# Performance work log

Measured on AMD Instinct MI355X. Metric: run time of the kernel, lower is better.

The kernel has to match this reference:

```python
import jax, jax.numpy as jnp
import numpy as np

Q_DIM = 9   # state(7) + action(2)
KV_DIM = 5  # fixed by get_input_tensors: 4 relative features + r_trans
H = 3
D = KV_DIM * H  # 15


def setup_inputs() -> dict:
    key = jax.random.key(0)
    ks = jax.random.split(key, 16)
    b, t = 32, 256

    def u(k, shape, fan_in):
        lim = (1.0 / fan_in) ** 0.5
        return jax.random.uniform(k, shape, jnp.float32, -lim, lim)

    return {
        "state": jax.random.normal(ks[0], (b, t, 7), jnp.float32),
        "action": jax.random.normal(ks[1], (b, t, 2), jnp.float32),
        "Wk": u(ks[2], (D, KV_DIM), KV_DIM),
        "Wq": u(ks[3], (D, Q_DIM), Q_DIM),
        "Wv": u(ks[4], (D, KV_DIM), KV_DIM),
        "att_bias": jax.random.uniform(ks[5], (KV_DIM,), jnp.float32, -0.1, 0.1),
        "Wscore": u(ks[6], (1, KV_DIM), KV_DIM),
        "bscore": u(ks[7], (1,), KV_DIM),
        "g1": jnp.ones((D,), jnp.float32),
        "beta1": jnp.zeros((D,), jnp.float32),
        "W1": u(ks[8], (5 * D, D), D),
        "bff1": u(ks[9], (5 * D,), D),
        "W2": u(ks[10], (D, 5 * D), 5 * D),
        "bff2": u(ks[11], (D,), 5 * D),
        "g2": jnp.ones((D,), jnp.float32),
        "beta2": jnp.zeros((D,), jnp.float32),
    }


def _layernorm(x, g, b, eps=1e-5):
    m = jnp.mean(x, axis=-1, keepdims=True)
    v = jnp.var(x, axis=-1, keepdims=True)
    return (x - m) * jax.lax.rsqrt(v + eps) * g + b


def _get_input_tensors(state):
    b, t, _ = state.shape
    init = state[..., :4]                                  # (b,t,4)
    rel = init[:, None, :, :] - init[:, :, None, :]        # (b,t,t,4): row i, col j -> s_j - s_i
    xy = rel.reshape(b, t, t, 2, 2).transpose(0, 1, 2, 4, 3)  # [...,0,:]=(x,vx), [...,1,:]=(y,vy)
    ang = -state[..., -1] + 0.5 * jnp.pi                   # (b,t)
    c = jnp.cos(ang)[:, None, :, None]                     # broadcast over row dim -> angle of col j
    s = jnp.sin(ang)[:, None, :, None]
    xr = xy[..., 0, :] * c - xy[..., 1, :] * s             # (b,t,t,2)
    yr = xy[..., 0, :] * s + xy[..., 1, :] * c
    rel = jnp.concatenate([xr, yr], axis=3)                # [xn,vxn,yn,vyn]
    rel = rel.reshape(b, t, t, 2, 2).transpose(0, 1, 2, 4, 3).reshape(b, t, t, 4)  # [xn,yn,vxn,vyn]
    # drop diagonal (j != i) via precomputed off-diagonal column indices
    rows = jnp.arange(t)[:, None]
    j = jnp.arange(t - 1)[None, :]
    cols = j + (j >= rows)                                 # (t,t-1)
    rel = rel[:, rows, cols, :]                            # (b,t,t-1,4)
    r = jnp.sqrt(rel[..., 0] ** 2 + rel[..., 1] ** 2)[..., None]  # (b,t,t-1,1)
    r_trans = 1.0 / (1.0 + jnp.exp(-1.0 + 5.0 * (r - 0.2)))
    kv_x = jnp.concatenate([rel[..., :2] / r, rel[..., 2:], r_trans], axis=-1)  # (b,t,t-1,5)
    return state, kv_x


def reference(state, action, Wk, Wq, Wv, att_bias, Wscore, bscore,
              g1, beta1, W1, bff1, W2, bff2, g2, beta2):
    q_x, kv_x = _get_input_tensors(state)
    q_x = jnp.concatenate([q_x, action], axis=-1)          # (b,t,Q_DIM)
    b, t, tm1, _ = kv_x.shape

    keys = (kv_x @ Wk.T).reshape(b, t, tm1, H, KV_DIM)     # (b,t,t-1,h,k)
    queries = (q_x @ Wq.T).reshape(b, t, 1, H, KV_DIM)
    e = jnp.tanh(keys + queries + att_bias)
    score = (e @ Wscore.T + bscore)[..., 0]                # (b,t,t-1,h)
    values = (kv_x @ Wv.T).reshape(b, t, tm1, H, KV_DIM)
    w = jax.nn.softmax(score, axis=2)                      # softmax over the t-1 neighbours
    x = jnp.einsum('btjh,btjhk->bthk', w, values).reshape(b, t, H * KV_DIM)

    x = _layernorm(x, g1, beta1)
    y = jax.nn.relu(x @ W1.T + bff1) @ W2.T + bff2
    x = x + y
    return _layernorm(x, g2, beta2)
```

## Files before the change

### kernel.cpp

```cpp
#include <hip/hip_runtime.h>
#include <math.h>

#define TT   256
#define TM1  255
#define QD   9
#define KD   5
#define NH   3
#define DD   15
#define HID  75
#define NR   18

#define K2E  2.8853900817779268f
#define L2E  1.4426950408889634f
#define INVK 0.34657359027997264f

typedef float v2f __attribute__((ext_vector_type(2)));

__device__ __forceinline__ v2f v2splat(float s) { v2f r; r.x = s; r.y = s; return r; }

__device__ __forceinline__ float fast_rcp(float x) {
    return __builtin_amdgcn_rcpf(x);
}

__device__ __forceinline__ float exp2_raw(float x) {
    float r; asm("v_exp_f32 %0, %1" : "=v"(r) : "v"(x)); return r;
}

template<int CTRL>
__device__ __forceinline__ float dpp_add(float x) {
    int y = __builtin_amdgcn_update_dpp(0, __float_as_int(x), CTRL, 0xf, 0xf, true);
    return x + __int_as_float(y);
}

__device__ __forceinline__ float wave_sum63(float x) {
    x = dpp_add<0x111>(x);
    x = dpp_add<0x112>(x);
    x = dpp_add<0x114>(x);
    x = dpp_add<0x118>(x);
    x = dpp_add<0x142>(x);
    x = dpp_add<0x143>(x);
    return x;
}

__device__ __forceinline__ float bcast(float x, int l) {
    return __int_as_float(__builtin_amdgcn_readlane(__float_as_int(x), l));
}

__global__ __launch_bounds__(256, 8)
void fused_block_kernel(const float* __restrict__ state,
                        const float* __restrict__ action,
                        const float* __restrict__ Wk,
                        const float* __restrict__ Wq,
                        const float* __restrict__ Wv,
                        const float* __restrict__ att_bias,
                        const float* __restrict__ Wscore,
                        const float* __restrict__ bscore,
                        const float* __restrict__ g1,
                        const float* __restrict__ beta1,
                        const float* __restrict__ W1,
                        const float* __restrict__ bff1,
                        const float* __restrict__ W2,
                        const float* __restrict__ bff2,
                        const float* __restrict__ g2,
                        const float* __restrict__ beta2,
                        float* __restrict__ out)
{
    const int tid  = threadIdx.x;
    const int lane = tid & 63;
    const int wv   = __builtin_amdgcn_readfirstlane(tid >> 6);
    const int qgrp = blockIdx.x * 4 + wv;
    const int b    = qgrp >> 8;
    const int qi   = qgrp & 255;

    __shared__ __align__(16) float s_wk8[DD*8];
    __shared__ float s_h[4][76];

    const float* __restrict__ sb  = state + (size_t)b*TT*7;
    const float* __restrict__ sti = sb + qi*7;
    const float si0 = sti[0], si1 = sti[1], si2 = sti[2], si3 = sti[3];

    if (tid < DD) {
        #pragma unroll
        for (int c = 0; c < KD; c++) s_wk8[tid*8+c] = Wk[tid*KD+c];
        s_wk8[tid*8+5] = -K2E * Wscore[tid % KD];
        s_wk8[tid*8+6] = 0.0f;
        s_wk8[tid*8+7] = 0.0f;
    }

    float qv = 0.0f;
    if (lane < DD) {
        float acc = att_bias[lane % KD];
        #pragma unroll
        for (int k = 0; k < 7; k++) acc = fmaf(Wq[lane*QD+k], sti[k], acc);
        acc = fmaf(Wq[lane*QD+7], action[((size_t)b*TT+qi)*2 + 0], acc);
        acc = fmaf(Wq[lane*QD+8], action[((size_t)b*TT+qi)*2 + 1], acc);
        qv = acc * K2E;
    }
    float qb2[DD];
    #pragma unroll
    for (int d = 0; d < DD; d++) qb2[d] = bcast(qv, d);

    float Cn = bscore[0];
    #pragma unroll
    for (int kk = 0; kk < KD; kk++) Cn += Wscore[kk];
    const float C2 = L2E * Cn;

    __syncthreads();

    float red[NR];
    #pragma unroll
    for (int n = 0; n < NR; n++) red[n] = 0.0f;

    #pragma unroll
    for (int g = 0; g < 2; g++) {
        const int mm0 = lane + g*128;
        const int mm1 = mm0 + 64;
        const int jj0 = mm0 + (mm0 >= qi ? 1 : 0);
        int       jj1 = mm1 + (mm1 >= qi ? 1 : 0);
        jj1 = (jj1 < TT) ? jj1 : (TT-1);
        const float* __restrict__ r0 = sb + jj0*7;
        const float* __restrict__ r1 = sb + jj1*7;

        v2f d0, d1, d2, d3, th;
        d0.x = r0[0]; d0.y = r1[0];
        d1.x = r0[1]; d1.y = r1[1];
        d2.x = r0[2]; d2.y = r1[2];
        d3.x = r0[3]; d3.y = r1[3];
        th.x = r0[6]; th.y = r1[6];
        d0 = d0 - v2splat(si0);
        d1 = d1 - v2splat(si1);
        d2 = d2 - v2splat(si2);
        d3 = d3 - v2splat(si3);

        v2f cs, sn;
        cs.x = __sinf(th.x); cs.y = __sinf(th.y);
        sn.x = __cosf(th.x); sn.y = __cosf(th.y);

        v2f xr0 = d0*cs - d1*sn;
        v2f yr0 = d0*sn + d1*cs;
        v2f xr1 = d2*cs - d3*sn;
        v2f yr1 = d2*sn + d3*cs;
        v2f s2  = xr0*xr0 + yr0*yr0;
        s2.x = fmaxf(s2.x, 1e-12f);
        s2.y = fmaxf(s2.y, 1e-12f);
        v2f rinv;
        rinv.x = __builtin_amdgcn_rsqf(s2.x);
        rinv.y = __builtin_amdgcn_rsqf(s2.y);
        v2f r = s2 * rinv;
        v2f ea;
        ea.x = exp2_raw(fmaf(7.213475204444817f, r.x, -2.8853900817779268f));
        ea.y = exp2_raw(fmaf(7.213475204444817f, r.y, -2.8853900817779268f));
        v2f rt;
        rt.x = fast_rcp(1.0f + ea.x);
        rt.y = fast_rcp(1.0f + ea.y);

        v2f t  = v2splat(K2E) * rinv;
        const v2f F0 = t * xr0;
        const v2f F1 = t * yr0;
        const v2f F2 = v2splat(K2E) * xr1;
        const v2f F3 = v2splat(K2E) * yr1;
        const v2f F4 = v2splat(K2E) * rt;

        v2f Cp;
        Cp.x = (mm0 < TM1) ? C2 : -100.0f;
        Cp.y = (mm1 < TM1) ? C2 : -100.0f;

        #pragma unroll
        for (int h = 0; h < NH; h++) {
            v2f sc = Cp;
            #pragma unroll
            for (int kk = 0; kk < KD; kk++) {
                const int d = h*KD + kk;
                const float4 wA = *(const float4*)&s_wk8[d*8];
                const float2 wB = *(const float2*)&s_wk8[d*8+4];

                v2f a = v2splat(qb2[d]);
                a = a + v2splat(wA.x) * F0;
                a = a + v2splat(wA.y) * F1;
                a = a + v2splat(wA.z) * F2;
                a = a + v2splat(wA.w) * F3;
                a = a + v2splat(wB.x) * F4;
                v2f e, sg;
                e.x = exp2_raw(a.x);
                e.y = exp2_raw(a.y);
                sg.x = fast_rcp(e.x + 1.0f);
                sg.y = fast_rcp(e.y + 1.0f);
                sc = sc + v2splat(wB.y) * sg;
            }
            v2f p;
            p.x = exp2_raw(sc.x);
            p.y = exp2_raw(sc.y);
            red[h] += p.x + p.y;
            red[NH+h*KD+0] = fmaf(p.y, F0.y, fmaf(p.x, F0.x, red[NH+h*KD+0]));
            red[NH+h*KD+1] = fmaf(p.y, F1.y, fmaf(p.x, F1.x, red[NH+h*KD+1]));
            red[NH+h*KD+2] = fmaf(p.y, F2.y, fmaf(p.x, F2.x, red[NH+h*KD+2]));
            red[NH+h*KD+3] = fmaf(p.y, F3.y, fmaf(p.x, F3.x, red[NH+h*KD+3]));
            red[NH+h*KD+4] = fmaf(p.y, F4.y, fmaf(p.x, F4.x, red[NH+h*KD+4]));
        }
    }

    #pragma unroll
    for (int n = 0; n < NR; n++) red[n] = wave_sum63(red[n]);
    float fin[NR];
    #pragma unroll
    for (int n = 0; n < NR; n++) fin[n] = bcast(red[n], 63);

    float xm = 0.0f;
    if (lane < DD) {
        const int h = lane / KD;
        float acc = 0.0f;
        #pragma unroll
        for (int c = 0; c < KD; c++) acc = fmaf(Wv[lane*KD+c], fin[NH+h*KD+c], acc);
        xm = acc * fast_rcp(fin[h]) * INVK;
    }

    float s1 = xm, sq = xm*xm;
    #pragma unroll
    for (int off = 8; off >= 1; off >>= 1) {
        s1 += __shfl_xor(s1, off, 16);
        sq += __shfl_xor(sq, off, 16);
    }
    const float mu1   = s1 * (1.0f/DD);
    const float rstd1 = rsqrtf(sq * (1.0f/DD) - mu1*mu1 + 1e-5f);
    float xln = 0.0f;
    if (lane < DD) xln = (xm - mu1) * rstd1 * g1[lane] + beta1[lane];

    float xs[DD];
    #pragma unroll
    for (int d = 0; d < DD; d++) xs[d] = bcast(xln, d);

    {
        float h0 = bff1[lane];
        #pragma unroll
        for (int k = 0; k < DD; k++) h0 = fmaf(W1[lane*DD+k], xs[k], h0);
        s_h[wv][lane] = fmaxf(h0, 0.0f);
        if (lane < HID-64) {
            float h1 = bff1[lane+64];
            #pragma unroll
            for (int k = 0; k < DD; k++) h1 = fmaf(W1[(lane+64)*DD+k], xs[k], h1);
            s_h[wv][lane+64] = fmaxf(h1, 0.0f);
        }
    }

    const int c2  = lane >> 4;
    const int d2c = lane & 15;
    const int cc  = (c2 < 3) ? c2 : 2;
    const int dc  = (d2c < DD) ? d2c : 0;
    float acc2 = 0.0f;
    #pragma unroll
    for (int k = 0; k < 25; k++)
        acc2 = fmaf(W2[dc*HID + cc*25 + k], s_h[wv][cc*25 + k], acc2);
    acc2 = (c2 < 3) ? acc2 : 0.0f;
    acc2 += __shfl_xor(acc2, 16);
    acc2 += __shfl_xor(acc2, 32);

    float x2 = 0.0f;
    if (lane < DD) x2 = xln + bff2[lane] + acc2;
    float t1 = x2, t2 = x2*x2;
    #pragma unroll
    for (int off = 8; off >= 1; off >>= 1) {
        t1 += __shfl_xor(t1, off, 16);
        t2 += __shfl_xor(t2, off, 16);
    }
    const float mu2   = t1 * (1.0f/DD);
    const float rstd2 = rsqrtf(t2 * (1.0f/DD) - mu2*mu2 + 1e-5f);
    if (lane < DD)
        out[(size_t)qgrp*DD + lane] = (x2 - mu2) * rstd2 * g2[lane] + beta2[lane];
}

extern "C" void kernel_launch(void* const* d_in, const int* in_sizes, int n_in,
                              void* d_out, int out_size, void* d_ws, size_t ws_size,
                              hipStream_t stream) {
    const float* state    = (const float*)d_in[0];
    const float* action   = (const float*)d_in[1];
    const float* Wk       = (const float*)d_in[2];
    const float* Wq       = (const float*)d_in[3];
    const float* Wv       = (const float*)d_in[4];
    const float* att_bias = (const float*)d_in[5];
    const float* Wscore   = (const float*)d_in[6];
    const float* bscore   = (const float*)d_in[7];
    const float* g1       = (const float*)d_in[8];
    const float* beta1    = (const float*)d_in[9];
    const float* W1       = (const float*)d_in[10];
    const float* bff1     = (const float*)d_in[11];
    const float* W2       = (const float*)d_in[12];
    const float* bff2     = (const float*)d_in[13];
    const float* g2       = (const float*)d_in[14];
    const float* beta2    = (const float*)d_in[15];
    float* out = (float*)d_out;

    dim3 grid(32 * 256 / 4);
    dim3 block(256);
    fused_block_kernel<<<grid, block, 0, stream>>>(
        state, action, Wk, Wq, Wv, att_bias, Wscore, bscore,
        g1, beta1, W1, bff1, W2, bff2, g2, beta2, out);
}
```

Measured before the change: 29.17 us.

## Split each query's neighbour loop across two waves with LDS reduction

New measurement: 29.28 us. About the same (+0.4%).

```diff
diff --git a/kernel.cpp b/kernel.cpp
--- a/kernel.cpp
+++ b/kernel.cpp
@@ -46,7 +46,7 @@
     return __int_as_float(__builtin_amdgcn_readlane(__float_as_int(x), l));
 }
 
-__global__ __launch_bounds__(256, 8)
+__global__ __launch_bounds__(256)
 void fused_block_kernel(const float* __restrict__ state,
                         const float* __restrict__ action,
                         const float* __restrict__ Wk,
@@ -68,12 +68,15 @@
     const int tid  = threadIdx.x;
     const int lane = tid & 63;
     const int wv   = __builtin_amdgcn_readfirstlane(tid >> 6);
-    const int qgrp = blockIdx.x * 4 + wv;
+    const int qloc = wv >> 1;
+    const int half = wv & 1;
+    const int qgrp = blockIdx.x * 2 + qloc;
     const int b    = qgrp >> 8;
     const int qi   = qgrp & 255;
 
     __shared__ __align__(16) float s_wk8[DD*8];
-    __shared__ float s_h[4][76];
+    __shared__ float s_red[2][2][NR];
+    __shared__ float s_h[2][76];
 
     const float* __restrict__ sb  = state + (size_t)b*TT*7;
     const float* __restrict__ sti = sb + qi*7;
@@ -107,13 +110,9 @@
 
     __syncthreads();
 
-    float red[NR];
-    #pragma unroll
-    for (int n = 0; n < NR; n++) red[n] = 0.0f;
-
-    #pragma unroll
-    for (int g = 0; g < 2; g++) {
-        const int mm0 = lane + g*128;
+    v2f F0, F1, F2, F3, F4, Cp;
+    {
+        const int mm0 = half*128 + lane;
         const int mm1 = mm0 + 64;
         const int jj0 = mm0 + (mm0 >= qi ? 1 : 0);
         int       jj1 = mm1 + (mm1 >= qi ? 1 : 0);
@@ -154,56 +153,67 @@
         rt.x = fast_rcp(1.0f + ea.x);
         rt.y = fast_rcp(1.0f + ea.y);
 
-        v2f t  = v2splat(K2E) * rinv;
-        const v2f F0 = t * xr0;
-        const v2f F1 = t * yr0;
-        const v2f F2 = v2splat(K2E) * xr1;
-        const v2f F3 = v2splat(K2E) * yr1;
-        const v2f F4 = v2splat(K2E) * rt;
-
-        v2f Cp;
+        v2f t = v2splat(K2E) * rinv;
+        F0 = t * xr0;
+        F1 = t * yr0;
+        F2 = v2splat(K2E) * xr1;
+        F3 = v2splat(K2E) * yr1;
+        F4 = v2splat(K2E) * rt;
+
         Cp.x = (mm0 < TM1) ? C2 : -100.0f;
         Cp.y = (mm1 < TM1) ? C2 : -100.0f;
-
-        #pragma unroll
-        for (int h = 0; h < NH; h++) {
-            v2f sc = Cp;
-            #pragma unroll
-            for (int kk = 0; kk < KD; kk++) {
-                const int d = h*KD + kk;
-                const float4 wA = *(const float4*)&s_wk8[d*8];
-                const float2 wB = *(const float2*)&s_wk8[d*8+4];
-
-                v2f a = v2splat(qb2[d]);
-                a = a + v2splat(wA.x) * F0;
-                a = a + v2splat(wA.y) * F1;
-                a = a + v2splat(wA.z) * F2;
-                a = a + v2splat(wA.w) * F3;
-                a = a + v2splat(wB.x) * F4;
-                v2f e, sg;
-                e.x = exp2_raw(a.x);
-                e.y = exp2_raw(a.y);
-                sg.x = fast_rcp(e.x + 1.0f);
-                sg.y = fast_rcp(e.y + 1.0f);
-                sc = sc + v2splat(wB.y) * sg;
-            }
-            v2f p;
-            p.x = exp2_raw(sc.x);
-            p.y = exp2_raw(sc.y);
-            red[h] += p.x + p.y;
-            red[NH+h*KD+0] = fmaf(p.y, F0.y, fmaf(p.x, F0.x, red[NH+h*KD+0]));
-            red[NH+h*KD+1] = fmaf(p.y, F1.y, fmaf(p.x, F1.x, red[NH+h*KD+1]));
-            red[NH+h*KD+2] = fmaf(p.y, F2.y, fmaf(p.x, F2.x, red[NH+h*KD+2]));
-            red[NH+h*KD+3] = fmaf(p.y, F3.y, fmaf(p.x, F3.x, red[NH+h*KD+3]));
-            red[NH+h*KD+4] = fmaf(p.y, F4.y, fmaf(p.x, F4.x, red[NH+h*KD+4]));
+    }
+
+    float red[NR];
+    #pragma unroll
+    for (int n = 0; n < NR; n++) red[n] = 0.0f;
+
+    #pragma unroll
+    for (int h = 0; h < NH; h++) {
+        v2f sc = Cp;
+        #pragma unroll
+        for (int kk = 0; kk < KD; kk++) {
+            const int d = h*KD + kk;
+            const float4 wA = *(const float4*)&s_wk8[d*8];
+            const float2 wB = *(const float2*)&s_wk8[d*8+4];
+
+            v2f a = v2splat(qb2[d]);
+            a = a + v2splat(wA.x) * F0;
+            a = a + v2splat(wA.y) * F1;
+            a = a + v2splat(wA.z) * F2;
+            a = a + v2splat(wA.w) * F3;
+            a = a + v2splat(wB.x) * F4;
+            v2f e, sg;
+            e.x = exp2_raw(a.x);
+            e.y = exp2_raw(a.y);
+            sg.x = fast_rcp(e.x + 1.0f);
+            sg.y = fast_rcp(e.y + 1.0f);
+            sc = sc + v2splat(wB.y) * sg;
         }
+        v2f p;
+        p.x = exp2_raw(sc.x);
+        p.y = exp2_raw(sc.y);
+        red[h] += p.x + p.y;
+        red[NH+h*KD+0] = fmaf(p.y, F0.y, fmaf(p.x, F0.x, red[NH+h*KD+0]));
+        red[NH+h*KD+1] = fmaf(p.y, F1.y, fmaf(p.x, F1.x, red[NH+h*KD+1]));
+        red[NH+h*KD+2] = fmaf(p.y, F2.y, fmaf(p.x, F2.x, red[NH+h*KD+2]));
+        red[NH+h*KD+3] = fmaf(p.y, F3.y, fmaf(p.x, F3.x, red[NH+h*KD+3]));
+        red[NH+h*KD+4] = fmaf(p.y, F4.y, fmaf(p.x, F4.x, red[NH+h*KD+4]));
     }
 
     #pragma unroll
     for (int n = 0; n < NR; n++) red[n] = wave_sum63(red[n]);
+    if (lane == 63) {
+        #pragma unroll
+        for (int n = 0; n < NR; n++) s_red[qloc][half][n] = red[n];
+    }
+    __syncthreads();
+    if (half == 1) return;
+
     float fin[NR];
     #pragma unroll
-    for (int n = 0; n < NR; n++) fin[n] = bcast(red[n], 63);
+    for (int n = 0; n < NR; n++)
+        fin[n] = s_red[qloc][0][n] + s_red[qloc][1][n];
 
     float xm = 0.0f;
     if (lane < DD) {
@@ -233,12 +243,12 @@
         float h0 = bff1[lane];
         #pragma unroll
         for (int k = 0; k < DD; k++) h0 = fmaf(W1[lane*DD+k], xs[k], h0);
-        s_h[wv][lane] = fmaxf(h0, 0.0f);
+        s_h[qloc][lane] = fmaxf(h0, 0.0f);
         if (lane < HID-64) {
             float h1 = bff1[lane+64];
             #pragma unroll
             for (int k = 0; k < DD; k++) h1 = fmaf(W1[(lane+64)*DD+k], xs[k], h1);
-            s_h[wv][lane+64] = fmaxf(h1, 0.0f);
+            s_h[qloc][lane+64] = fmaxf(h1, 0.0f);
         }
     }
 
@@ -249,7 +259,7 @@
     float acc2 = 0.0f;
     #pragma unroll
     for (int k = 0; k < 25; k++)
-        acc2 = fmaf(W2[dc*HID + cc*25 + k], s_h[wv][cc*25 + k], acc2);
+        acc2 = fmaf(W2[dc*HID + cc*25 + k], s_h[qloc][cc*25 + k], acc2);
     acc2 = (c2 < 3) ? acc2 : 0.0f;
     acc2 += __shfl_xor(acc2, 16);
     acc2 += __shfl_xor(acc2, 32);
@@ -289,7 +299,7 @@
     const float* beta2    = (const float*)d_in[15];
     float* out = (float*)d_out;
 
-    dim3 grid(32 * 256 / 4);
+    dim3 grid(32 * 256 / 2);
     dim3 block(256);
     fused_block_kernel<<<grid, block, 0, stream>>>(
         state, action, Wk, Wq, Wv, att_bias, Wscore, bscore,
```
